# Optimization experiments

Measured on AMD Instinct MI355X. Metric: run time of the kernel, lower is better.

Reference implementation:

```python
import jax, jax.numpy as jnp
import numpy as np

# Static ragged block structure: (num_graphs_in_bucket, n) -> block tensor (B, n, n, C)
BLOCKS = [(128, 32), (64, 48), (32, 64), (16, 96)]
C = 64
DEPTH = 2
EPS = 1e-5
N_TOTAL = sum(b * n * n for b, n in BLOCKS)  # 557056


def _mlp(h, w, b):
    # stack of DEPTH Linear(C->C) + ReLU layers (1x1 convs in the torch module)
    for d in range(w.shape[0]):
        h = jax.nn.relu(jnp.einsum('...i,oi->...o', h, w[d]) + b[d])
    return h


def _bn(h, g, b, m, v):
    # eval-mode BatchNorm1d with running stats
    return g * (h - m) * jax.lax.rsqrt(v + EPS) + b


def setup_inputs() -> dict:
    key = jax.random.key(0)
    ks = jax.random.split(key, 8)
    s = 1.0 / np.sqrt(C)

    def lin(k):
        return jax.random.normal(k, (C, C), jnp.float32) * s

    return dict(
        x=jax.random.normal(ks[0], (N_TOTAL, C), jnp.float32),
        w_m1=jax.random.normal(ks[1], (DEPTH, C, C), jnp.float32) * s,
        b_m1=jnp.zeros((DEPTH, C), jnp.float32),
        w_m2=jax.random.normal(ks[2], (DEPTH, C, C), jnp.float32) * s,
        b_m2=jnp.zeros((DEPTH, C), jnp.float32),
        W_skip=lin(ks[3]), b_skip=jnp.zeros((C,), jnp.float32),
        W_u1=lin(ks[4]), b_u1=jnp.zeros((C,), jnp.float32),
        g1=jnp.ones((C,), jnp.float32), beta1=jnp.zeros((C,), jnp.float32),
        rm1=jnp.zeros((C,), jnp.float32), rv1=jnp.ones((C,), jnp.float32),
        W_u2=lin(ks[5]), b_u2=jnp.zeros((C,), jnp.float32),
        g2=jnp.ones((C,), jnp.float32), beta2=jnp.zeros((C,), jnp.float32),
        rm2=jnp.zeros((C,), jnp.float32), rv2=jnp.ones((C,), jnp.float32),
    )


def reference(x, w_m1, b_m1, w_m2, b_m2, W_skip, b_skip,
              W_u1, b_u1, g1, beta1, rm1, rv1,
              W_u2, b_u2, g2, beta2, rm2, rv2):
    # --- ragged split -> per-block PPGN-style matmul conv -> cat ---
    hs = []
    off = 0
    for (bnum, n) in BLOCKS:
        ln = bnum * n * n
        blk = x[off:off + ln].reshape(bnum, n, n, C)  # (B, n, n, C)
        m1 = _mlp(blk, w_m1, b_m1)
        m2 = _mlp(blk, w_m2, b_m2)
        # per-channel spatial matmul over the n x n block
        h = jnp.einsum('bijc,bjkc->bikc', m1, m2)
        hs.append(h.reshape(ln, C))
        off += ln
    hs2 = jnp.concatenate(hs, 0) + (x @ W_skip.T + b_skip)
    # --- update MLP: Linear-BN-ReLU-(Dropout eval=id)-Linear-BN-ReLU + residual ---
    u = jax.nn.relu(_bn(hs2 @ W_u1.T + b_u1, g1, beta1, rm1, rv1))
    u = jax.nn.relu(_bn(u @ W_u2.T + b_u2, g2, beta2, rm2, rv2))
    return u + hs2
```

## Files before the change

### kernel.cpp

```cpp
#include <hip/hip_runtime.h>
#include <hip/hip_bf16.h>

#define NT 557056
typedef __hip_bfloat16 bf16;
typedef __attribute__((ext_vector_type(8))) short short8;
typedef __attribute__((ext_vector_type(4))) short short4v;
typedef __attribute__((ext_vector_type(4))) float f32x4;

__device__ __forceinline__ float b2f(bf16 v){ return __bfloat162float(v); }
__device__ __forceinline__ short f2bs(float f){ bf16 h = __float2bfloat16(f); return *(short*)&h; }
__device__ __forceinline__ float s2f(short s){ bf16 h = *(bf16*)&s; return __bfloat162float(h); }

__device__ __forceinline__ short8 cvt8(float4 a, float4 b){
  short8 r;
  r[0]=f2bs(a.x); r[1]=f2bs(a.y); r[2]=f2bs(a.z); r[3]=f2bs(a.w);
  r[4]=f2bs(b.x); r[5]=f2bs(b.y); r[6]=f2bs(b.z); r[7]=f2bs(b.w);
  return r;
}
__device__ __forceinline__ short8 ldfrag(const float* __restrict__ p){
  return cvt8(*(const float4*)p, *(const float4*)(p + 4));
}
#define MFMA(a,b,c) __builtin_amdgcn_mfma_f32_16x16x32_bf16(a, b, c, 0, 0, 0)
#define LGKM0() asm volatile("s_waitcnt lgkmcnt(0)" ::: "memory")

__global__ __launch_bounds__(256, 2) void k1_mlp(
    const float* __restrict__ x,
    const float* __restrict__ w_m1, const float* __restrict__ b_m1,
    const float* __restrict__ w_m2, const float* __restrict__ b_m2,
    bf16* __restrict__ m1t, bf16* __restrict__ m2t)
{
  __shared__ short yL[4][16][72];
  const int tid = threadIdx.x;
  const int wv = tid >> 6, lane = tid & 63, r = lane & 15, g = lane >> 4;
  const int wid = blockIdx.x * 4 + wv;

  short8 wf[4][4][2];
  {
    const float* wp0 = w_m1;         const float* wp1 = w_m1 + 4096;
    const float* wp2 = w_m2;         const float* wp3 = w_m2 + 4096;
    #pragma unroll
    for (int cb = 0; cb < 4; ++cb)
      #pragma unroll
      for (int s = 0; s < 2; ++s) {
        const int o = (cb*16 + r)*64 + s*32 + g*8;
        wf[0][cb][s] = ldfrag(wp0 + o);
        wf[1][cb][s] = ldfrag(wp1 + o);
        wf[2][cb][s] = ldfrag(wp2 + o);
        wf[3][cb][s] = ldfrag(wp3 + o);
      }
  }
  f32x4 b0v[2][4];
  float b1v[2][4];
  #pragma unroll
  for (int m = 0; m < 2; ++m) {
    const float* bb = m ? b_m2 : b_m1;
    #pragma unroll
    for (int cb = 0; cb < 4; ++cb) {
      b0v[m][cb] = *(const f32x4*)(bb + cb*16 + 4*g);
      b1v[m][cb] = bb[64 + cb*16 + r];
    }
  }

  size_t pb = (size_t)wid * (17*16);
  const float* xp0 = x + (pb + r)*64 + g*8;
  float4 xr0 = *(const float4*)(xp0);
  float4 xr1 = *(const float4*)(xp0 + 4);
  float4 xr2 = *(const float4*)(xp0 + 32);
  float4 xr3 = *(const float4*)(xp0 + 36);

  for (int t = 0; t < 17; ++t, pb += 16) {
    short8 xf0 = cvt8(xr0, xr1);
    short8 xf1 = cvt8(xr2, xr3);
    if (t < 16) {
      const float* xn = x + (pb + 16 + r)*64 + g*8;
      xr0 = *(const float4*)(xn);
      xr1 = *(const float4*)(xn + 4);
      xr2 = *(const float4*)(xn + 32);
      xr3 = *(const float4*)(xn + 36);
    }
    #pragma unroll
    for (int m = 0; m < 2; ++m) {
      f32x4 acc[4];
      #pragma unroll
      for (int cb = 0; cb < 4; ++cb) acc[cb] = b0v[m][cb];
      #pragma unroll
      for (int cb = 0; cb < 4; ++cb) {
        acc[cb] = MFMA(wf[2*m][cb][0], xf0, acc[cb]);
        acc[cb] = MFMA(wf[2*m][cb][1], xf1, acc[cb]);
      }
      #pragma unroll
      for (int cb = 0; cb < 4; ++cb) {
        short4v v;
        #pragma unroll
        for (int q = 0; q < 4; ++q) v[q] = f2bs(fmaxf(acc[cb][q], 0.f));
        *(short4v*)&yL[wv][r][cb*16 + 4*g] = v;
      }
      LGKM0();
      short8 a0 = *(const short8*)&yL[wv][r][g*8];
      short8 a1 = *(const short8*)&yL[wv][r][32 + g*8];
      f32x4 acc2[4];
      #pragma unroll
      for (int cb = 0; cb < 4; ++cb) {
        const float bv = b1v[m][cb];
        acc2[cb] = (f32x4){bv, bv, bv, bv};
      }
      #pragma unroll
      for (int cb = 0; cb < 4; ++cb) {
        acc2[cb] = MFMA(a0, wf[2*m+1][cb][0], acc2[cb]);
        acc2[cb] = MFMA(a1, wf[2*m+1][cb][1], acc2[cb]);
      }
      bf16* op = m ? m2t : m1t;
      #pragma unroll
      for (int cb = 0; cb < 4; ++cb) {
        short4v v;
        #pragma unroll
        for (int q = 0; q < 4; ++q) v[q] = f2bs(fmaxf(acc2[cb][q], 0.f));
        *(short4v*)(op + (size_t)(cb*16 + r) * NT + pb + 4*g) = v;
      }
    }
  }
}

template<int N>
__global__ __launch_bounds__(256) void k2_spatial(
    const bf16* __restrict__ m1t, const bf16* __restrict__ m2t,
    bf16* __restrict__ ht, int off)
{
  constexpr int T = N / 16;
  constexpr int SA = N + 4;
  __shared__ __align__(16) float AT[N*SA];
  __shared__ __align__(16) float Bs[N*SA];
  const int b = blockIdx.x >> 6;
  const int c = blockIdx.x & 63;
  const size_t pbase = (size_t)c * NT + (size_t)off + (size_t)b * N * N;
  const int tid = threadIdx.x;

  for (int idx = tid*4; idx < N*N; idx += 1024) {
    short4v a4 = *(const short4v*)(m1t + pbase + idx);
    short4v b4 = *(const short4v*)(m2t + pbase + idx);
    const int j = idx / N, k0 = idx - j*N;
    f32x4 bf;
    #pragma unroll
    for (int q = 0; q < 4; ++q) bf[q] = s2f(b4[q]);
    *(f32x4*)&Bs[j*SA + k0] = bf;
    #pragma unroll
    for (int q = 0; q < 4; ++q) AT[(k0+q)*SA + j] = s2f(a4[q]);
  }
  __syncthreads();

  const int ti = tid >> 4, tk = tid & 15;
  float acc[T][T];
  #pragma unroll
  for (int ii = 0; ii < T; ++ii)
    #pragma unroll
    for (int kk = 0; kk < T; ++kk) acc[ii][kk] = 0.f;

  for (int j = 0; j < N; ++j) {
    const float* ar = &AT[j*SA + ti*T];
    const float* br = &Bs[j*SA + tk*T];
    float av[T], bv[T];
    if constexpr (T == 2) {
      float2 a2 = *(const float2*)ar; av[0]=a2.x; av[1]=a2.y;
      float2 b2 = *(const float2*)br; bv[0]=b2.x; bv[1]=b2.y;
    } else if constexpr (T == 3) {
      av[0]=ar[0]; av[1]=ar[1]; av[2]=ar[2];
      bv[0]=br[0]; bv[1]=br[1]; bv[2]=br[2];
    } else if constexpr (T == 4) {
      float4 a4 = *(const float4*)ar; av[0]=a4.x; av[1]=a4.y; av[2]=a4.z; av[3]=a4.w;
      float4 b4 = *(const float4*)br; bv[0]=b4.x; bv[1]=b4.y; bv[2]=b4.z; bv[3]=b4.w;
    } else {
      #pragma unroll
      for (int p = 0; p < 3; ++p) {
        float2 a2 = *(const float2*)(ar + 2*p); av[2*p]=a2.x; av[2*p+1]=a2.y;
        float2 b2 = *(const float2*)(br + 2*p); bv[2*p]=b2.x; bv[2*p+1]=b2.y;
      }
    }
    #pragma unroll
    for (int ii = 0; ii < T; ++ii)
      #pragma unroll
      for (int kk = 0; kk < T; ++kk)
        acc[ii][kk] = fmaf(av[ii], bv[kk], acc[ii][kk]);
  }

  #pragma unroll
  for (int ii = 0; ii < T; ++ii) {
    const int row = ti*T + ii;
    bf16* dst = ht + pbase + row*N + tk*T;
    unsigned short tmp[T];
    #pragma unroll
    for (int kk = 0; kk < T; ++kk) tmp[kk] = (unsigned short)f2bs(acc[ii][kk]);
    if constexpr (T == 2) {
      *(unsigned int*)dst = (unsigned int)tmp[0] | ((unsigned int)tmp[1] << 16);
    } else if constexpr (T == 3) {
      ((unsigned short*)dst)[0] = tmp[0];
      ((unsigned short*)dst)[1] = tmp[1];
      ((unsigned short*)dst)[2] = tmp[2];
    } else if constexpr (T == 4) {
      short4v v; v[0]=(short)tmp[0]; v[1]=(short)tmp[1]; v[2]=(short)tmp[2]; v[3]=(short)tmp[3];
      *(short4v*)dst = v;
    } else {
      #pragma unroll
      for (int p = 0; p < 3; ++p)
        *((unsigned int*)dst + p) = (unsigned int)tmp[2*p] | ((unsigned int)tmp[2*p+1] << 16);
    }
  }
}

__global__ __launch_bounds__(256, 2) void k3_update(
    const float* __restrict__ x, const bf16* __restrict__ ht,
    const float* __restrict__ Wskip, const float* __restrict__ bskip,
    const float* __restrict__ Wu1, const float* __restrict__ bu1,
    const float* __restrict__ g1, const float* __restrict__ be1,
    const float* __restrict__ rm1, const float* __restrict__ rv1,
    const float* __restrict__ Wu2, const float* __restrict__ bu2,
    const float* __restrict__ g2, const float* __restrict__ be2,
    const float* __restrict__ rm2, const float* __restrict__ rv2,
    float* __restrict__ out)
{
  __shared__ short hs2L[4][16][88];
  __shared__ short u1L[4][16][72];
  const int tid = threadIdx.x;
  const int wv = tid >> 6, lane = tid & 63, r = lane & 15, g = lane >> 4;
  const int wid = blockIdx.x * 4 + wv;

  short8 wsk[4][2], w1f[4][2], w2f[4][2];
  #pragma unroll
  for (int cb = 0; cb < 4; ++cb)
    #pragma unroll
    for (int s = 0; s < 2; ++s) {
      const int o = (cb*16 + r)*64 + s*32 + g*8;
      wsk[cb][s] = ldfrag(Wskip + o);
      w1f[cb][s] = ldfrag(Wu1 + o);
      w2f[cb][s] = ldfrag(Wu2 + o);
    }
  float bskv[4];
  f32x4 sc1v[4], sh1v[4], sc2v[4], sh2v[4];
  #pragma unroll
  for (int cb = 0; cb < 4; ++cb) {
    bskv[cb] = bskip[cb*16 + r];
    const int o = cb*16 + 4*g;
    f32x4 gg1 = *(const f32x4*)(g1 + o),  vv1 = *(const f32x4*)(rv1 + o);
    f32x4 mm1 = *(const f32x4*)(rm1 + o), bb1 = *(const f32x4*)(be1 + o);
    f32x4 bu1v = *(const f32x4*)(bu1 + o);
    f32x4 gg2 = *(const f32x4*)(g2 + o),  vv2 = *(const f32x4*)(rv2 + o);
    f32x4 mm2 = *(const f32x4*)(rm2 + o), bb2 = *(const f32x4*)(be2 + o);
    f32x4 bu2v = *(const f32x4*)(bu2 + o);
    #pragma unroll
    for (int q = 0; q < 4; ++q) {
      const float s1 = gg1[q] * rsqrtf(vv1[q] + 1e-5f);
      sc1v[cb][q] = s1; sh1v[cb][q] = bb1[q] + (bu1v[q] - mm1[q]) * s1;
      const float s2 = gg2[q] * rsqrtf(vv2[q] + 1e-5f);
      sc2v[cb][q] = s2; sh2v[cb][q] = bb2[q] + (bu2v[q] - mm2[q]) * s2;
    }
  }

  size_t pb = (size_t)wid * (17*16);
  const float* xp0 = x + (pb + r)*64 + g*8;
  float4 xr0 = *(const float4*)(xp0);
  float4 xr1 = *(const float4*)(xp0 + 4);
  float4 xr2 = *(const float4*)(xp0 + 32);
  float4 xr3 = *(const float4*)(xp0 + 36);

  for (int t = 0; t < 17; ++t, pb += 16) {
    short8 xf0 = cvt8(xr0, xr1);
    short8 xf1 = cvt8(xr2, xr3);
    if (t < 16) {
      const float* xn = x + (pb + 16 + r)*64 + g*8;
      xr0 = *(const float4*)(xn);
      xr1 = *(const float4*)(xn + 4);
      xr2 = *(const float4*)(xn + 32);
      xr3 = *(const float4*)(xn + 36);
    }
    short4v hv[4];
    #pragma unroll
    for (int cb = 0; cb < 4; ++cb)
      hv[cb] = *(const short4v*)(ht + (size_t)(cb*16 + r) * NT + pb + 4*g);

    f32x4 acc[4];
    #pragma unroll
    for (int cb = 0; cb < 4; ++cb) acc[cb] = (f32x4){bskv[cb], bskv[cb], bskv[cb], bskv[cb]};
    #pragma unroll
    for (int cb = 0; cb < 4; ++cb) {
      acc[cb] = MFMA(xf0, wsk[cb][0], acc[cb]);
      acc[cb] = MFMA(xf1, wsk[cb][1], acc[cb]);
    }
    #pragma unroll
    for (int cb = 0; cb < 4; ++cb)
      #pragma unroll
      for (int q = 0; q < 4; ++q) acc[cb][q] += s2f(hv[cb][q]);
    #pragma unroll
    for (int cb = 0; cb < 4; ++cb)
      #pragma unroll
      for (int q = 0; q < 4; ++q)
        hs2L[wv][4*g + q][cb*16 + r] = f2bs(acc[cb][q]);
    LGKM0();
    short8 h0 = *(const short8*)&hs2L[wv][r][g*8];
    short8 h1 = *(const short8*)&hs2L[wv][r][32 + g*8];

    f32x4 a1[4];
    #pragma unroll
    for (int cb = 0; cb < 4; ++cb) a1[cb] = (f32x4){0.f, 0.f, 0.f, 0.f};
    #pragma unroll
    for (int cb = 0; cb < 4; ++cb) {
      a1[cb] = MFMA(w1f[cb][0], h0, a1[cb]);
      a1[cb] = MFMA(w1f[cb][1], h1, a1[cb]);
    }
    #pragma unroll
    for (int cb = 0; cb < 4; ++cb) {
      short4v v;
      #pragma unroll
      for (int q = 0; q < 4; ++q)
        v[q] = f2bs(fmaxf(a1[cb][q]*sc1v[cb][q] + sh1v[cb][q], 0.f));
      *(short4v*)&u1L[wv][r][cb*16 + 4*g] = v;
    }
    LGKM0();
    short8 u0 = *(const short8*)&u1L[wv][r][g*8];
    short8 u1f = *(const short8*)&u1L[wv][r][32 + g*8];

    f32x4 a2[4];
    #pragma unroll
    for (int cb = 0; cb < 4; ++cb) a2[cb] = (f32x4){0.f, 0.f, 0.f, 0.f};
    #pragma unroll
    for (int cb = 0; cb < 4; ++cb) {
      a2[cb] = MFMA(w2f[cb][0], u0, a2[cb]);
      a2[cb] = MFMA(w2f[cb][1], u1f, a2[cb]);
    }
    #pragma unroll
    for (int cb = 0; cb < 4; ++cb) {
      short4v hres = *(const short4v*)&hs2L[wv][r][cb*16 + 4*g];
      f32x4 res;
      #pragma unroll
      for (int q = 0; q < 4; ++q)
        res[q] = fmaxf(a2[cb][q]*sc2v[cb][q] + sh2v[cb][q], 0.f) + s2f(hres[q]);
      *(f32x4*)(out + (pb + r)*64 + cb*16 + 4*g) = res;
    }
  }
}

extern "C" void kernel_launch(void* const* d_in, const int* in_sizes, int n_in,
                              void* d_out, int out_size, void* d_ws, size_t ws_size,
                              hipStream_t stream) {
  const float* x     = (const float*)d_in[0];
  const float* w_m1  = (const float*)d_in[1];
  const float* b_m1  = (const float*)d_in[2];
  const float* w_m2  = (const float*)d_in[3];
  const float* b_m2  = (const float*)d_in[4];
  const float* Wskip = (const float*)d_in[5];
  const float* bskip = (const float*)d_in[6];
  const float* Wu1   = (const float*)d_in[7];
  const float* bu1   = (const float*)d_in[8];
  const float* g1    = (const float*)d_in[9];
  const float* be1   = (const float*)d_in[10];
  const float* rm1   = (const float*)d_in[11];
  const float* rv1   = (const float*)d_in[12];
  const float* Wu2   = (const float*)d_in[13];
  const float* bu2   = (const float*)d_in[14];
  const float* g2    = (const float*)d_in[15];
  const float* be2   = (const float*)d_in[16];
  const float* rm2   = (const float*)d_in[17];
  const float* rv2   = (const float*)d_in[18];
  float* out = (float*)d_out;

  bf16* m1t = (bf16*)d_ws;
  bf16* m2t = m1t + (size_t)64 * NT;
  bf16* ht  = m1t;

  k1_mlp<<<512, 256, 0, stream>>>(x, w_m1, b_m1, w_m2, b_m2, m1t, m2t);

  k2_spatial<32><<<128*64, 256, 0, stream>>>(m1t, m2t, ht, 0);
  k2_spatial<48><<< 64*64, 256, 0, stream>>>(m1t, m2t, ht, 131072);
  k2_spatial<64><<< 32*64, 256, 0, stream>>>(m1t, m2t, ht, 278528);
  k2_spatial<96><<< 16*64, 256, 0, stream>>>(m1t, m2t, ht, 409600);

  k3_update<<<512, 256, 0, stream>>>(x, ht, Wskip, bskip,
                                     Wu1, bu1, g1, be1, rm1, rv1,
                                     Wu2, bu2, g2, be2, rm2, rv2, out);
}
```

Before: 566.2 us.

## Process 32 rows per wave iteration and fold BN scale into weights

In both pointwise kernels, each wave now handles two 16-row tiles per iteration instead of one, and work is spread across more blocks (1088 instead of 512, 128 rows per wave). This raises MFMA-level parallelism per wave and increases grid occupancy. The update kernel also folds the eval-mode BatchNorm scale into the bf16 weights and uses the folded shift as the accumulator init, which removes per-element multiply-adds. The explicit lgkmcnt waits are dropped. The trade-offs are higher register pressure, and slightly different rounding because the scaled weights are rounded to bf16.

```diff
diff --git a/kernel.cpp b/kernel.cpp
--- a/kernel.cpp
+++ b/kernel.cpp
@@ -7,7 +7,6 @@
 typedef __attribute__((ext_vector_type(4))) short short4v;
 typedef __attribute__((ext_vector_type(4))) float f32x4;
 
-__device__ __forceinline__ float b2f(bf16 v){ return __bfloat162float(v); }
 __device__ __forceinline__ short f2bs(float f){ bf16 h = __float2bfloat16(f); return *(short*)&h; }
 __device__ __forceinline__ float s2f(short s){ bf16 h = *(bf16*)&s; return __bfloat162float(h); }
 
@@ -20,8 +19,14 @@
 __device__ __forceinline__ short8 ldfrag(const float* __restrict__ p){
   return cvt8(*(const float4*)p, *(const float4*)(p + 4));
 }
+__device__ __forceinline__ short8 ldfrag_s(const float* __restrict__ p, float s){
+  float4 a = *(const float4*)p, b = *(const float4*)(p + 4);
+  a.x*=s; a.y*=s; a.z*=s; a.w*=s; b.x*=s; b.y*=s; b.z*=s; b.w*=s;
+  return cvt8(a, b);
+}
 #define MFMA(a,b,c) __builtin_amdgcn_mfma_f32_16x16x32_bf16(a, b, c, 0, 0, 0)
-#define LGKM0() asm volatile("s_waitcnt lgkmcnt(0)" ::: "memory")
+
+#define LS 88
 
 __global__ __launch_bounds__(256, 2) void k1_mlp(
     const float* __restrict__ x,
@@ -29,26 +34,22 @@
     const float* __restrict__ w_m2, const float* __restrict__ b_m2,
     bf16* __restrict__ m1t, bf16* __restrict__ m2t)
 {
-  __shared__ short yL[4][16][72];
+  __shared__ short yL[4][2][32][LS];
   const int tid = threadIdx.x;
   const int wv = tid >> 6, lane = tid & 63, r = lane & 15, g = lane >> 4;
   const int wid = blockIdx.x * 4 + wv;
 
   short8 wf[4][4][2];
-  {
-    const float* wp0 = w_m1;         const float* wp1 = w_m1 + 4096;
-    const float* wp2 = w_m2;         const float* wp3 = w_m2 + 4096;
-    #pragma unroll
-    for (int cb = 0; cb < 4; ++cb)
-      #pragma unroll
-      for (int s = 0; s < 2; ++s) {
-        const int o = (cb*16 + r)*64 + s*32 + g*8;
-        wf[0][cb][s] = ldfrag(wp0 + o);
-        wf[1][cb][s] = ldfrag(wp1 + o);
-        wf[2][cb][s] = ldfrag(wp2 + o);
-        wf[3][cb][s] = ldfrag(wp3 + o);
-      }
-  }
+  #pragma unroll
+  for (int cb = 0; cb < 4; ++cb)
+    #pragma unroll
+    for (int s = 0; s < 2; ++s) {
+      const int o = (cb*16 + r)*64 + s*32 + g*8;
+      wf[0][cb][s] = ldfrag(w_m1 + o);
+      wf[1][cb][s] = ldfrag(w_m1 + 4096 + o);
+      wf[2][cb][s] = ldfrag(w_m2 + o);
+      wf[3][cb][s] = ldfrag(w_m2 + 4096 + o);
+    }
   f32x4 b0v[2][4];
   float b1v[2][4];
   #pragma unroll
@@ -61,62 +62,83 @@
     }
   }
 
-  size_t pb = (size_t)wid * (17*16);
-  const float* xp0 = x + (pb + r)*64 + g*8;
-  float4 xr0 = *(const float4*)(xp0);
-  float4 xr1 = *(const float4*)(xp0 + 4);
-  float4 xr2 = *(const float4*)(xp0 + 32);
-  float4 xr3 = *(const float4*)(xp0 + 36);
-
-  for (int t = 0; t < 17; ++t, pb += 16) {
-    short8 xf0 = cvt8(xr0, xr1);
-    short8 xf1 = cvt8(xr2, xr3);
-    if (t < 16) {
-      const float* xn = x + (pb + 16 + r)*64 + g*8;
-      xr0 = *(const float4*)(xn);
-      xr1 = *(const float4*)(xn + 4);
-      xr2 = *(const float4*)(xn + 32);
-      xr3 = *(const float4*)(xn + 36);
+  size_t pb = (size_t)wid * 128;
+
+  float4 xr[8];
+  #pragma unroll
+  for (int h = 0; h < 2; ++h) {
+    const float* xp = x + (pb + h*16 + r)*64 + g*8;
+    xr[4*h+0] = *(const float4*)(xp);
+    xr[4*h+1] = *(const float4*)(xp + 4);
+    xr[4*h+2] = *(const float4*)(xp + 32);
+    xr[4*h+3] = *(const float4*)(xp + 36);
+  }
+
+  for (int t = 0; t < 4; ++t, pb += 32) {
+    short8 xf[2][2];
+    xf[0][0] = cvt8(xr[0], xr[1]);  xf[0][1] = cvt8(xr[2], xr[3]);
+    xf[1][0] = cvt8(xr[4], xr[5]);  xf[1][1] = cvt8(xr[6], xr[7]);
+    if (t < 3) {
+      #pragma unroll
+      for (int h = 0; h < 2; ++h) {
+        const float* xp = x + (pb + 32 + h*16 + r)*64 + g*8;
+        xr[4*h+0] = *(const float4*)(xp);
+        xr[4*h+1] = *(const float4*)(xp + 4);
+        xr[4*h+2] = *(const float4*)(xp + 32);
+        xr[4*h+3] = *(const float4*)(xp + 36);
+      }
     }
     #pragma unroll
     for (int m = 0; m < 2; ++m) {
-      f32x4 acc[4];
-      #pragma unroll
-      for (int cb = 0; cb < 4; ++cb) acc[cb] = b0v[m][cb];
-      #pragma unroll
-      for (int cb = 0; cb < 4; ++cb) {
-        acc[cb] = MFMA(wf[2*m][cb][0], xf0, acc[cb]);
-        acc[cb] = MFMA(wf[2*m][cb][1], xf1, acc[cb]);
-      }
-      #pragma unroll
-      for (int cb = 0; cb < 4; ++cb) {
-        short4v v;
-        #pragma unroll
-        for (int q = 0; q < 4; ++q) v[q] = f2bs(fmaxf(acc[cb][q], 0.f));
-        *(short4v*)&yL[wv][r][cb*16 + 4*g] = v;
-      }
-      LGKM0();
-      short8 a0 = *(const short8*)&yL[wv][r][g*8];
-      short8 a1 = *(const short8*)&yL[wv][r][32 + g*8];
-      f32x4 acc2[4];
+      f32x4 acc[4][2];
+      #pragma unroll
+      for (int cb = 0; cb < 4; ++cb) { acc[cb][0] = b0v[m][cb]; acc[cb][1] = b0v[m][cb]; }
+      #pragma unroll
+      for (int cb = 0; cb < 4; ++cb)
+        #pragma unroll
+        for (int s = 0; s < 2; ++s) {
+          acc[cb][0] = MFMA(wf[2*m][cb][s], xf[0][s], acc[cb][0]);
+          acc[cb][1] = MFMA(wf[2*m][cb][s], xf[1][s], acc[cb][1]);
+        }
+      #pragma unroll
+      for (int cb = 0; cb < 4; ++cb)
+        #pragma unroll
+        for (int th = 0; th < 2; ++th) {
+          short4v v;
+          #pragma unroll
+          for (int q = 0; q < 4; ++q) v[q] = f2bs(fmaxf(acc[cb][th][q], 0.f));
+          *(short4v*)&yL[wv][m][th*16 + r][cb*16 + 4*g] = v;
+        }
+      short8 af[2][2];
+      #pragma unroll
+      for (int th = 0; th < 2; ++th)
+        #pragma unroll
+        for (int s = 0; s < 2; ++s)
+          af[th][s] = *(const short8*)&yL[wv][m][th*16 + r][s*32 + g*8];
+      f32x4 acc2[4][2];
       #pragma unroll
       for (int cb = 0; cb < 4; ++cb) {
         const float bv = b1v[m][cb];
-        acc2[cb] = (f32x4){bv, bv, bv, bv};
-      }
-      #pragma unroll
-      for (int cb = 0; cb < 4; ++cb) {
-        acc2[cb] = MFMA(a0, wf[2*m+1][cb][0], acc2[cb]);
-        acc2[cb] = MFMA(a1, wf[2*m+1][cb][1], acc2[cb]);
-      }
+        acc2[cb][0] = (f32x4){bv,bv,bv,bv};
+        acc2[cb][1] = (f32x4){bv,bv,bv,bv};
+      }
+      #pragma unroll
+      for (int cb = 0; cb < 4; ++cb)
+        #pragma unroll
+        for (int s = 0; s < 2; ++s) {
+          acc2[cb][0] = MFMA(af[0][s], wf[2*m+1][cb][s], acc2[cb][0]);
+          acc2[cb][1] = MFMA(af[1][s], wf[2*m+1][cb][s], acc2[cb][1]);
+        }
       bf16* op = m ? m2t : m1t;
       #pragma unroll
-      for (int cb = 0; cb < 4; ++cb) {
-        short4v v;
-        #pragma unroll
-        for (int q = 0; q < 4; ++q) v[q] = f2bs(fmaxf(acc2[cb][q], 0.f));
-        *(short4v*)(op + (size_t)(cb*16 + r) * NT + pb + 4*g) = v;
-      }
+      for (int cb = 0; cb < 4; ++cb)
+        #pragma unroll
+        for (int th = 0; th < 2; ++th) {
+          short4v v;
+          #pragma unroll
+          for (int q = 0; q < 4; ++q) v[q] = f2bs(fmaxf(acc2[cb][th][q], 0.f));
+          *(short4v*)(op + (size_t)(cb*16 + r) * NT + pb + th*16 + 4*g) = v;
+        }
     }
   }
 }
@@ -217,123 +239,157 @@
     const float* __restrict__ rm2, const float* __restrict__ rv2,
     float* __restrict__ out)
 {
-  __shared__ short hs2L[4][16][88];
-  __shared__ short u1L[4][16][72];
+  __shared__ short hs2L[4][32][LS];
+  __shared__ short u1L[4][32][LS];
   const int tid = threadIdx.x;
   const int wv = tid >> 6, lane = tid & 63, r = lane & 15, g = lane >> 4;
   const int wid = blockIdx.x * 4 + wv;
 
   short8 wsk[4][2], w1f[4][2], w2f[4][2];
-  #pragma unroll
-  for (int cb = 0; cb < 4; ++cb)
+  float bskv[4];
+  f32x4 b1c[4], b2c[4];
+  #pragma unroll
+  for (int cb = 0; cb < 4; ++cb) {
+    const int row = cb*16 + r;
+    const float s1 = g1[row] * rsqrtf(rv1[row] + 1e-5f);
+    const float s2 = g2[row] * rsqrtf(rv2[row] + 1e-5f);
     #pragma unroll
     for (int s = 0; s < 2; ++s) {
-      const int o = (cb*16 + r)*64 + s*32 + g*8;
+      const int o = row*64 + s*32 + g*8;
       wsk[cb][s] = ldfrag(Wskip + o);
-      w1f[cb][s] = ldfrag(Wu1 + o);
-      w2f[cb][s] = ldfrag(Wu2 + o);
-    }
-  float bskv[4];
-  f32x4 sc1v[4], sh1v[4], sc2v[4], sh2v[4];
-  #pragma unroll
-  for (int cb = 0; cb < 4; ++cb) {
-    bskv[cb] = bskip[cb*16 + r];
-    const int o = cb*16 + 4*g;
-    f32x4 gg1 = *(const f32x4*)(g1 + o),  vv1 = *(const f32x4*)(rv1 + o);
-    f32x4 mm1 = *(const f32x4*)(rm1 + o), bb1 = *(const f32x4*)(be1 + o);
-    f32x4 bu1v = *(const f32x4*)(bu1 + o);
-    f32x4 gg2 = *(const f32x4*)(g2 + o),  vv2 = *(const f32x4*)(rv2 + o);
-    f32x4 mm2 = *(const f32x4*)(rm2 + o), bb2 = *(const f32x4*)(be2 + o);
-    f32x4 bu2v = *(const f32x4*)(bu2 + o);
+      w1f[cb][s] = ldfrag_s(Wu1 + o, s1);
+      w2f[cb][s] = ldfrag_s(Wu2 + o, s2);
+    }
+    bskv[cb] = bskip[row];
+    const int o4 = cb*16 + 4*g;
+    f32x4 gg1 = *(const f32x4*)(g1 + o4),  vv1 = *(const f32x4*)(rv1 + o4);
+    f32x4 mm1 = *(const f32x4*)(rm1 + o4), bb1 = *(const f32x4*)(be1 + o4);
+    f32x4 u1b = *(const f32x4*)(bu1 + o4);
+    f32x4 gg2 = *(const f32x4*)(g2 + o4),  vv2 = *(const f32x4*)(rv2 + o4);
+    f32x4 mm2 = *(const f32x4*)(rm2 + o4), bb2 = *(const f32x4*)(be2 + o4);
+    f32x4 u2b = *(const f32x4*)(bu2 + o4);
     #pragma unroll
     for (int q = 0; q < 4; ++q) {
-      const float s1 = gg1[q] * rsqrtf(vv1[q] + 1e-5f);
-      sc1v[cb][q] = s1; sh1v[cb][q] = bb1[q] + (bu1v[q] - mm1[q]) * s1;
-      const float s2 = gg2[q] * rsqrtf(vv2[q] + 1e-5f);
-      sc2v[cb][q] = s2; sh2v[cb][q] = bb2[q] + (bu2v[q] - mm2[q]) * s2;
-    }
-  }
-
-  size_t pb = (size_t)wid * (17*16);
-  const float* xp0 = x + (pb + r)*64 + g*8;
-  float4 xr0 = *(const float4*)(xp0);
-  float4 xr1 = *(const float4*)(xp0 + 4);
-  float4 xr2 = *(const float4*)(xp0 + 32);
-  float4 xr3 = *(const float4*)(xp0 + 36);
-
-  for (int t = 0; t < 17; ++t, pb += 16) {
-    short8 xf0 = cvt8(xr0, xr1);
-    short8 xf1 = cvt8(xr2, xr3);
-    if (t < 16) {
-      const float* xn = x + (pb + 16 + r)*64 + g*8;
-      xr0 = *(const float4*)(xn);
-      xr1 = *(const float4*)(xn + 4);
-      xr2 = *(const float4*)(xn + 32);
-      xr3 = *(const float4*)(xn + 36);
-    }
-    short4v hv[4];
-    #pragma unroll
-    for (int cb = 0; cb < 4; ++cb)
-      hv[cb] = *(const short4v*)(ht + (size_t)(cb*16 + r) * NT + pb + 4*g);
-
-    f32x4 acc[4];
-    #pragma unroll
-    for (int cb = 0; cb < 4; ++cb) acc[cb] = (f32x4){bskv[cb], bskv[cb], bskv[cb], bskv[cb]};
+      const float c1 = gg1[q] * rsqrtf(vv1[q] + 1e-5f);
+      b1c[cb][q] = bb1[q] + (u1b[q] - mm1[q]) * c1;
+      const float c2 = gg2[q] * rsqrtf(vv2[q] + 1e-5f);
+      b2c[cb][q] = bb2[q] + (u2b[q] - mm2[q]) * c2;
+    }
+  }
+
+  size_t pb = (size_t)wid * 128;
+
+  float4 xr[8];
+  #pragma unroll
+  for (int h = 0; h < 2; ++h) {
+    const float* xp = x + (pb + h*16 + r)*64 + g*8;
+    xr[4*h+0] = *(const float4*)(xp);
+    xr[4*h+1] = *(const float4*)(xp + 4);
+    xr[4*h+2] = *(const float4*)(xp + 32);
+    xr[4*h+3] = *(const float4*)(xp + 36);
+  }
+
+  for (int t = 0; t < 4; ++t, pb += 32) {
+    short8 xf[2][2];
+    xf[0][0] = cvt8(xr[0], xr[1]);  xf[0][1] = cvt8(xr[2], xr[3]);
+    xf[1][0] = cvt8(xr[4], xr[5]);  xf[1][1] = cvt8(xr[6], xr[7]);
+    if (t < 3) {
+      #pragma unroll
+      for (int h = 0; h < 2; ++h) {
+        const float* xp = x + (pb + 32 + h*16 + r)*64 + g*8;
+        xr[4*h+0] = *(const float4*)(xp);
+        xr[4*h+1] = *(const float4*)(xp + 4);
+        xr[4*h+2] = *(const float4*)(xp + 32);
+        xr[4*h+3] = *(const float4*)(xp + 36);
+      }
+    }
+    short4v hv[4][2];
+    #pragma unroll
+    for (int cb = 0; cb < 4; ++cb)
+      #pragma unroll
+      for (int th = 0; th < 2; ++th)
+        hv[cb][th] = *(const short4v*)(ht + (size_t)(cb*16 + r) * NT + pb + th*16 + 4*g);
+
+    f32x4 acc[4][2];
     #pragma unroll
     for (int cb = 0; cb < 4; ++cb) {
-      acc[cb] = MFMA(xf0, wsk[cb][0], acc[cb]);
-      acc[cb] = MFMA(xf1, wsk[cb][1], acc[cb]);
-    }
-    #pragma unroll
-    for (int cb = 0; cb < 4; ++cb)
-      #pragma unroll
-      for (int q = 0; q < 4; ++q) acc[cb][q] += s2f(hv[cb][q]);
-    #pragma unroll
-    for (int cb = 0; cb < 4; ++cb)
-      #pragma unroll
-      for (int q = 0; q < 4; ++q)
-        hs2L[wv][4*g + q][cb*16 + r] = f2bs(acc[cb][q]);
-    LGKM0();
-    short8 h0 = *(const short8*)&hs2L[wv][r][g*8];
-    short8 h1 = *(const short8*)&hs2L[wv][r][32 + g*8];
-
-    f32x4 a1[4];
-    #pragma unroll
-    for (int cb = 0; cb < 4; ++cb) a1[cb] = (f32x4){0.f, 0.f, 0.f, 0.f};
-    #pragma unroll
-    for (int cb = 0; cb < 4; ++cb) {
-      a1[cb] = MFMA(w1f[cb][0], h0, a1[cb]);
-      a1[cb] = MFMA(w1f[cb][1], h1, a1[cb]);
-    }
-    #pragma unroll
-    for (int cb = 0; cb < 4; ++cb) {
-      short4v v;
-      #pragma unroll
-      for (int q = 0; q < 4; ++q)
-        v[q] = f2bs(fmaxf(a1[cb][q]*sc1v[cb][q] + sh1v[cb][q], 0.f));
-      *(short4v*)&u1L[wv][r][cb*16 + 4*g] = v;
-    }
-    LGKM0();
-    short8 u0 = *(const short8*)&u1L[wv][r][g*8];
-    short8 u1f = *(const short8*)&u1L[wv][r][32 + g*8];
-
-    f32x4 a2[4];
-    #pragma unroll
-    for (int cb = 0; cb < 4; ++cb) a2[cb] = (f32x4){0.f, 0.f, 0.f, 0.f};
-    #pragma unroll
-    for (int cb = 0; cb < 4; ++cb) {
-      a2[cb] = MFMA(w2f[cb][0], u0, a2[cb]);
-      a2[cb] = MFMA(w2f[cb][1], u1f, a2[cb]);
-    }
-    #pragma unroll
-    for (int cb = 0; cb < 4; ++cb) {
-      short4v hres = *(const short4v*)&hs2L[wv][r][cb*16 + 4*g];
-      f32x4 res;
-      #pragma unroll
-      for (int q = 0; q < 4; ++q)
-        res[q] = fmaxf(a2[cb][q]*sc2v[cb][q] + sh2v[cb][q], 0.f) + s2f(hres[q]);
-      *(f32x4*)(out + (pb + r)*64 + cb*16 + 4*g) = res;
-    }
+      acc[cb][0] = (f32x4){bskv[cb], bskv[cb], bskv[cb], bskv[cb]};
+      acc[cb][1] = acc[cb][0];
+    }
+    #pragma unroll
+    for (int cb = 0; cb < 4; ++cb)
+      #pragma unroll
+      for (int s = 0; s < 2; ++s) {
+        acc[cb][0] = MFMA(xf[0][s], wsk[cb][s], acc[cb][0]);
+        acc[cb][1] = MFMA(xf[1][s], wsk[cb][s], acc[cb][1]);
+      }
+    #pragma unroll
+    for (int cb = 0; cb < 4; ++cb)
+      #pragma unroll
+      for (int th = 0; th < 2; ++th)
+        #pragma unroll
+        for (int q = 0; q < 4; ++q) acc[cb][th][q] += s2f(hv[cb][th][q]);
+    #pragma unroll
+    for (int cb = 0; cb < 4; ++cb)
+      #pragma unroll
+      for (int th = 0; th < 2; ++th)
+        #pragma unroll
+        for (int q = 0; q < 4; ++q)
+          hs2L[wv][th*16 + 4*g + q][cb*16 + r] = f2bs(acc[cb][th][q]);
+    short8 hf[2][2];
+    #pragma unroll
+    for (int th = 0; th < 2; ++th)
+      #pragma unroll
+      for (int s = 0; s < 2; ++s)
+        hf[th][s] = *(const short8*)&hs2L[wv][th*16 + r][s*32 + g*8];
+
+    f32x4 a1[4][2];
+    #pragma unroll
+    for (int cb = 0; cb < 4; ++cb) { a1[cb][0] = b1c[cb]; a1[cb][1] = b1c[cb]; }
+    #pragma unroll
+    for (int cb = 0; cb < 4; ++cb)
+      #pragma unroll
+      for (int s = 0; s < 2; ++s) {
+        a1[cb][0] = MFMA(w1f[cb][s], hf[0][s], a1[cb][0]);
+        a1[cb][1] = MFMA(w1f[cb][s], hf[1][s], a1[cb][1]);
+      }
+    #pragma unroll
+    for (int cb = 0; cb < 4; ++cb)
+      #pragma unroll
+      for (int th = 0; th < 2; ++th) {
+        short4v v;
+        #pragma unroll
+        for (int q = 0; q < 4; ++q) v[q] = f2bs(fmaxf(a1[cb][th][q], 0.f));
+        *(short4v*)&u1L[wv][th*16 + r][cb*16 + 4*g] = v;
+      }
+    short8 uf[2][2];
+    #pragma unroll
+    for (int th = 0; th < 2; ++th)
+      #pragma unroll
+      for (int s = 0; s < 2; ++s)
+        uf[th][s] = *(const short8*)&u1L[wv][th*16 + r][s*32 + g*8];
+
+    f32x4 a2[4][2];
+    #pragma unroll
+    for (int cb = 0; cb < 4; ++cb) { a2[cb][0] = b2c[cb]; a2[cb][1] = b2c[cb]; }
+    #pragma unroll
+    for (int cb = 0; cb < 4; ++cb)
+      #pragma unroll
+      for (int s = 0; s < 2; ++s) {
+        a2[cb][0] = MFMA(w2f[cb][s], uf[0][s], a2[cb][0]);
+        a2[cb][1] = MFMA(w2f[cb][s], uf[1][s], a2[cb][1]);
+      }
+    #pragma unroll
+    for (int cb = 0; cb < 4; ++cb)
+      #pragma unroll
+      for (int th = 0; th < 2; ++th) {
+        short4v hres = *(const short4v*)&hs2L[wv][th*16 + r][cb*16 + 4*g];
+        f32x4 res;
+        #pragma unroll
+        for (int q = 0; q < 4; ++q)
+          res[q] = fmaxf(a2[cb][th][q], 0.f) + s2f(hres[q]);
+        *(f32x4*)(out + (pb + th*16 + r)*64 + cb*16 + 4*g) = res;
+      }
   }
 }
 
@@ -365,14 +421,14 @@
   bf16* m2t = m1t + (size_t)64 * NT;
   bf16* ht  = m1t;
 
-  k1_mlp<<<512, 256, 0, stream>>>(x, w_m1, b_m1, w_m2, b_m2, m1t, m2t);
+  k1_mlp<<<1088, 256, 0, stream>>>(x, w_m1, b_m1, w_m2, b_m2, m1t, m2t);
 
   k2_spatial<32><<<128*64, 256, 0, stream>>>(m1t, m2t, ht, 0);
   k2_spatial<48><<< 64*64, 256, 0, stream>>>(m1t, m2t, ht, 131072);
   k2_spatial<64><<< 32*64, 256, 0, stream>>>(m1t, m2t, ht, 278528);
   k2_spatial<96><<< 16*64, 256, 0, stream>>>(m1t, m2t, ht, 409600);
 
-  k3_update<<<512, 256, 0, stream>>>(x, ht, Wskip, bskip,
-                                     Wu1, bu1, g1, be1, rm1, rv1,
-                                     Wu2, bu2, g2, be2, rm2, rv2, out);
-}
+  k3_update<<<1088, 256, 0, stream>>>(x, ht, Wskip, bskip,
+                                      Wu1, bu1, g1, be1, rm1, rv1,
+                                      Wu2, bu2, g2, be2, rm2, rv2, out);
+}
```

Measured after the change: 557.4 us. About the same (-1.6%).
